# Performance work log

Measured on AMD Instinct MI355X. Metric: run time of the kernel, lower is better.

## Reference

```python
import jax, jax.numpy as jnp
import numpy as np

FORGET_BIAS = 1.0

def _lstm_step(c, h, x, W, b):
    # TF BasicLSTMCell: gates = [x; h] @ W + b, split order i, j, f, o
    z = jnp.concatenate([x, h], axis=-1) @ W + b
    i, j, f, o = jnp.split(z, 4, axis=-1)
    c_new = c * jax.nn.sigmoid(f + FORGET_BIAS) + jax.nn.sigmoid(i) * jnp.tanh(j)
    h_new = jnp.tanh(c_new) * jax.nn.sigmoid(o)
    return c_new, h_new


def setup_inputs() -> dict:
    key = jax.random.key(0)
    ks = jax.random.split(key, 8)
    V, B, T, H = 32000, 32, 256, 256
    input_data = jax.random.randint(ks[0], (B, T), 0, V, dtype=jnp.int64)
    targets = jax.random.randint(ks[1], (B, T), 0, V, dtype=jnp.int64)
    embedding = jax.random.uniform(ks[2], (V, H), jnp.float32, -1.0, 1.0)
    s = 1.0 / np.sqrt(2 * H)
    W1 = jax.random.normal(ks[3], (2 * H, 4 * H), jnp.float32) * s
    b1 = jnp.zeros((4 * H,), jnp.float32)
    W2 = jax.random.normal(ks[4], (2 * H, 4 * H), jnp.float32) * s
    b2 = jnp.zeros((4 * H,), jnp.float32)
    softmax_w = jax.random.normal(ks[5], (H, V), jnp.float32) * (1.0 / np.sqrt(H))
    softmax_b = jnp.zeros((V,), jnp.float32)
    return {"input_data": input_data, "targets": targets, "embedding": embedding,
            "W1": W1, "b1": b1, "W2": W2, "b2": b2,
            "softmax_w": softmax_w, "softmax_b": softmax_b}


def reference(input_data, targets, embedding, W1, b1, W2, b2, softmax_w, softmax_b):
    B, T = input_data.shape
    H = embedding.shape[1]
    xs = embedding[input_data].transpose(1, 0, 2)  # [T, B, H]

    def step(carry, x):
        c1, h1, c2, h2 = carry
        c1, h1 = _lstm_step(c1, h1, x, W1, b1)
        c2, h2 = _lstm_step(c2, h2, h1, W2, b2)
        return (c1, h1, c2, h2), h2

    z = jnp.zeros((B, H), xs.dtype)
    _, hs = jax.lax.scan(step, (z, z, z, z), xs)  # hs: [T, B, H]
    out = hs.transpose(1, 0, 2).reshape(-1, H)    # batch-major flatten, matches tf concat(1,...)
    logits = out @ softmax_w + softmax_b          # [B*T, V]
    logp = jax.nn.log_softmax(logits, axis=-1)
    tgt = targets.reshape(-1)
    loss = -jnp.take_along_axis(logp, tgt[:, None], axis=1)[:, 0]  # [B*T]
    cost = jnp.sum(loss) / B / T
    return cost
```

## Files before the change

kernel.cpp:

```cpp
#include <hip/hip_runtime.h>
#include <hip/hip_bf16.h>

#define Vv 32000
#define Tz 256
#define Hz 256

typedef __attribute__((ext_vector_type(8))) short short8;
typedef __attribute__((ext_vector_type(4))) float f32x4;

__device__ __forceinline__ float sigm(float x) { return 1.f / (1.f + __expf(-x)); }
__device__ __forceinline__ unsigned short f2bf(float x) {
    union { __hip_bfloat16 h; unsigned short u; } cv; cv.h = __float2bfloat16(x); return cv.u;
}

__global__ __launch_bounds__(256) void k_swt(const float* __restrict__ sw,
                                             __hip_bfloat16* __restrict__ swt) {
    __shared__ float tile[64][65];
    int kt = blockIdx.x & 3, vt = blockIdx.x >> 2;
    int k0 = kt * 64, v0 = vt * 64, tid = threadIdx.x;
#pragma unroll
    for (int p = 0; p < 16; ++p) {
        int lin = p * 256 + tid;
        int kk = lin >> 6, vvi = lin & 63;
        tile[kk][vvi] = sw[(size_t)(k0 + kk) * Vv + v0 + vvi];
    }
    __syncthreads();
#pragma unroll
    for (int p = 0; p < 16; ++p) {
        int lin = p * 256 + tid;
        int vvi = lin >> 6, kk = lin & 63;
        swt[(size_t)(v0 + vvi) * 256 + k0 + kk] = __float2bfloat16(tile[kk][vvi]);
    }
}

__global__ __launch_bounds__(64) void k_embed(const int* __restrict__ inp,
    const float* __restrict__ emb, __hip_bfloat16* __restrict__ xs) {
    int row = blockIdx.x;
    int t = row >> 5, b = row & 31;
    const float* src = emb + (size_t)inp[b * Tz + t] * Hz;
    int tid = threadIdx.x;
    float4 v = *(const float4*)&src[tid * 4];
    __hip_bfloat16* dst = xs + (size_t)row * Hz + tid * 4;
    dst[0] = __float2bfloat16(v.x); dst[1] = __float2bfloat16(v.y);
    dst[2] = __float2bfloat16(v.z); dst[3] = __float2bfloat16(v.w);
}

__device__ __forceinline__ void grid_barrier(unsigned* cnt) {
    __syncthreads();
    if (threadIdx.x == 0) {
        unsigned ticket = __hip_atomic_fetch_add(cnt, 1u, __ATOMIC_RELEASE, __HIP_MEMORY_SCOPE_AGENT);
        unsigned target = (ticket / 64u + 1u) * 64u;
        while (__hip_atomic_load(cnt, __ATOMIC_ACQUIRE, __HIP_MEMORY_SCOPE_AGENT) < target)
            __builtin_amdgcn_s_sleep(8);
    }
    __syncthreads();
}

__global__ __launch_bounds__(256) void k_lstm(
    const __hip_bfloat16* __restrict__ xs,
    const float* __restrict__ W1, const float* __restrict__ b1v,
    const float* __restrict__ W2, const float* __restrict__ b2v,
    __hip_bfloat16* __restrict__ h1buf,
    __hip_bfloat16* __restrict__ h2buf,
    float* __restrict__ houtF, __hip_bfloat16* __restrict__ houtB,
    unsigned* __restrict__ cnt)
{
    __shared__ __align__(16) unsigned short Wl[32 * 528];
    __shared__ __align__(16) unsigned short inh[32 * 272];
    __shared__ float zl[32 * 33];
    __shared__ float c_l[256];

    int bid = blockIdx.x;
    int which = bid >> 5;
    int bp = bid & 31;
    int nb = bp * 8;
    int tid = threadIdx.x;
    int w = tid >> 6, l = tid & 63, lr = l & 15, lk = l >> 4;

    const float* W    = which ? W2 : W1;
    const float* bptr = which ? b2v : b1v;

    {
        int u = tid & 31, klane = tid >> 5;
        int zc = ((u >> 3) << 8) + nb + (u & 7);
#pragma unroll 8
        for (int it = 0; it < 64; ++it) {
            int k = klane + it * 8;
            Wl[u * 528 + k] = f2bf(W[(size_t)k * 1024 + zc]);
        }
    }
    c_l[tid] = 0.f;
    float bfrag;
    {
        int r = ((w & 1) << 4) + lr;
        bfrag = bptr[((r >> 3) << 8) + nb + (r & 7)];
    }
    __syncthreads();

    float* zbuf = (float*)inh;

    for (int node = 0; node <= 256; ++node) {
        int t = which ? (node - 1) : node;
        bool valid = which ? (t >= 0) : (t < 256);
        if (valid) {
            f32x4 acc[2][2];
#pragma unroll
            for (int m = 0; m < 2; ++m)
#pragma unroll
                for (int n = 0; n < 2; ++n) acc[m][n] = (f32x4){0.f, 0.f, 0.f, 0.f};

            const unsigned short* h1p = (const unsigned short*)h1buf + ((node - 1) & 1) * 8192;
#pragma unroll
            for (int kh = 0; kh < 2; ++kh) {
                const unsigned short* src;
                if (!which) src = kh ? h1p : (const unsigned short*)xs + (size_t)t * 8192;
                else        src = kh ? (const unsigned short*)h2buf + (node & 1) * 8192 : h1p;
#pragma unroll
                for (int i = 0; i < 4; ++i) {
                    int fi = i * 256 + tid;
                    int b = fi >> 5, seg = fi & 31;
                    *(short8*)&inh[b * 272 + seg * 8] = *(const short8*)&src[fi * 8];
                }
                __syncthreads();
#pragma unroll
                for (int s = 0; s < 2; ++s) {
                    int kl = w * 64 + s * 32;
                    short8 a0 = *(const short8*)&inh[lr * 272 + kl + lk * 8];
                    short8 a1 = *(const short8*)&inh[(16 + lr) * 272 + kl + lk * 8];
                    short8 q0 = *(const short8*)&Wl[lr * 528 + kh * 256 + kl + lk * 8];
                    short8 q1 = *(const short8*)&Wl[(16 + lr) * 528 + kh * 256 + kl + lk * 8];
                    acc[0][0] = __builtin_amdgcn_mfma_f32_16x16x32_bf16(a0, q0, acc[0][0], 0, 0, 0);
                    acc[0][1] = __builtin_amdgcn_mfma_f32_16x16x32_bf16(a0, q1, acc[0][1], 0, 0, 0);
                    acc[1][0] = __builtin_amdgcn_mfma_f32_16x16x32_bf16(a1, q0, acc[1][0], 0, 0, 0);
                    acc[1][1] = __builtin_amdgcn_mfma_f32_16x16x32_bf16(a1, q1, acc[1][1], 0, 0, 0);
                }
                __syncthreads();
            }
#pragma unroll
            for (int m = 0; m < 2; ++m)
#pragma unroll
                for (int n = 0; n < 2; ++n)
                    *(f32x4*)&zbuf[((w * 4 + m * 2 + n) * 64 + l) * 4] = acc[m][n];
            __syncthreads();
            {
                int m = w >> 1, n = w & 1;
                f32x4 z = (f32x4){0.f, 0.f, 0.f, 0.f};
#pragma unroll
                for (int wv = 0; wv < 4; ++wv)
                    z += *(const f32x4*)&zbuf[((wv * 4 + m * 2 + n) * 64 + l) * 4];
                int r = n * 16 + lr;
#pragma unroll
                for (int j = 0; j < 4; ++j) {
                    int b = m * 16 + lk * 4 + j;
                    zl[b * 33 + r] = z[j] + bfrag;
                }
            }
            __syncthreads();
            {
                int jj = tid & 7, b = tid >> 3;
                float zi = zl[b * 33 + jj];
                float zj = zl[b * 33 + 8 + jj];
                float zf = zl[b * 33 + 16 + jj];
                float zo = zl[b * 33 + 24 + jj];
                float c = c_l[tid];
                float cn = c * sigm(zf + 1.f) + sigm(zi) * tanhf(zj);
                c_l[tid] = cn;
                float hv = tanhf(cn) * sigm(zo);
                int col = nb + jj;
                if (!which) {
                    ((unsigned short*)h1buf)[(node & 1) * 8192 + b * 256 + col] = f2bf(hv);
                } else {
                    ((unsigned short*)h2buf)[((node - 1) & 1) * 8192 + b * 256 + col] = f2bf(hv);
                    size_t row = (size_t)b * Tz + t;
                    houtF[row * 256 + col] = hv;
                    ((unsigned short*)houtB)[row * 256 + col] = f2bf(hv);
                }
            }
        }
        grid_barrier(cnt);
    }
}

__global__ __launch_bounds__(256) void k_gemm(const __hip_bfloat16* __restrict__ Abf,
    const __hip_bfloat16* __restrict__ Bbf, const float* __restrict__ sb,
    float* __restrict__ row_sum)
{
    __shared__ __align__(16) unsigned short As[128 * 64];
    __shared__ __align__(16) unsigned short Bs[128 * 64];
    int tid = threadIdx.x;
    size_t r0 = (size_t)blockIdx.x * 128;
    size_t c0 = (size_t)blockIdx.y * 128;
    int l = tid & 63, w = tid >> 6, lr = l & 15, lk = l >> 4;

    f32x4 acc[2][8];
#pragma unroll
    for (int m = 0; m < 2; ++m)
#pragma unroll
        for (int f = 0; f < 8; ++f) acc[m][f] = (f32x4){0.f, 0.f, 0.f, 0.f};

    const unsigned short* A = (const unsigned short*)Abf;
    const unsigned short* B = (const unsigned short*)Bbf;

    for (int kt = 0; kt < 4; ++kt) {
#pragma unroll
        for (int i = 0; i < 4; ++i) {
            int fi = i * 256 + tid;
            int row = fi >> 3, seg = fi & 7;
            int dseg = seg ^ (row & 7);
            *(short8*)&As[row * 64 + dseg * 8] =
                *(const short8*)&A[(r0 + row) * 256 + kt * 64 + seg * 8];
            *(short8*)&Bs[row * 64 + dseg * 8] =
                *(const short8*)&B[(c0 + row) * 256 + kt * 64 + seg * 8];
        }
        __syncthreads();
#pragma unroll
        for (int ks = 0; ks < 2; ++ks) {
            short8 a[2];
#pragma unroll
            for (int m = 0; m < 2; ++m) {
                int row = w * 32 + m * 16 + lr;
                a[m] = *(const short8*)&As[row * 64 + ((ks * 4 + lk) ^ (row & 7)) * 8];
            }
#pragma unroll
            for (int f = 0; f < 8; ++f) {
                int row = f * 16 + lr;
                short8 bfr = *(const short8*)&Bs[row * 64 + ((ks * 4 + lk) ^ (row & 7)) * 8];
#pragma unroll
                for (int m = 0; m < 2; ++m)
                    acc[m][f] = __builtin_amdgcn_mfma_f32_16x16x32_bf16(a[m], bfr, acc[m][f], 0, 0, 0);
            }
        }
        __syncthreads();
    }

    float sums[2][4] = {{0.f,0.f,0.f,0.f},{0.f,0.f,0.f,0.f}};
#pragma unroll
    for (int f = 0; f < 8; ++f) {
        float sbv = sb[c0 + f * 16 + lr];
#pragma unroll
        for (int m = 0; m < 2; ++m)
#pragma unroll
            for (int j = 0; j < 4; ++j) sums[m][j] += __expf(acc[m][f][j] + sbv);
    }
#pragma unroll
    for (int msk = 1; msk <= 8; msk <<= 1)
#pragma unroll
        for (int m = 0; m < 2; ++m)
#pragma unroll
            for (int j = 0; j < 4; ++j) sums[m][j] += __shfl_xor(sums[m][j], msk);
    if (lr == 0) {
#pragma unroll
        for (int m = 0; m < 2; ++m)
#pragma unroll
            for (int j = 0; j < 4; ++j)
                atomicAdd(&row_sum[r0 + w * 32 + m * 16 + lk * 4 + j], sums[m][j]);
    }
}

__global__ __launch_bounds__(256) void k_loss(const float* __restrict__ houtF,
    const float* __restrict__ sw, const float* __restrict__ sb,
    const int* __restrict__ tgts, const float* __restrict__ row_sum,
    float* __restrict__ out)
{
    int r = blockIdx.x * 256 + threadIdx.x;
    int tg = tgts[r];
    const float* h = houtF + (size_t)r * Hz;
    const float* wp = sw + tg;
    float acc = 0.f;
#pragma unroll 8
    for (int k = 0; k < Hz; ++k) acc += h[k] * wp[(size_t)k * Vv];
    float loss = logf(row_sum[r]) - (acc + sb[tg]);
#pragma unroll
    for (int m = 1; m < 64; m <<= 1) loss += __shfl_xor(loss, m);
    __shared__ float red[4];
    int l = threadIdx.x & 63, wv = threadIdx.x >> 6;
    if (l == 0) red[wv] = loss;
    __syncthreads();
    if (threadIdx.x == 0) {
        float s = red[0] + red[1] + red[2] + red[3];
        atomicAdd(out, s * (1.f / 8192.f));
    }
}

extern "C" void kernel_launch(void* const* d_in, const int* in_sizes, int n_in,
                              void* d_out, int out_size, void* d_ws, size_t ws_size,
                              hipStream_t stream)
{
    const int*   inp = (const int*)d_in[0];
    const int*   tgt = (const int*)d_in[1];
    const float* emb = (const float*)d_in[2];
    const float* W1  = (const float*)d_in[3];
    const float* b1  = (const float*)d_in[4];
    const float* W2  = (const float*)d_in[5];
    const float* b2  = (const float*)d_in[6];
    const float* sw  = (const float*)d_in[7];
    const float* sb  = (const float*)d_in[8];
    float* out = (float*)d_out;

    char* ws = (char*)d_ws;
    size_t off = 0;
    __hip_bfloat16* SWT  = (__hip_bfloat16*)(ws + off); off += (size_t)Vv * Hz * 2;
    __hip_bfloat16* XS   = (__hip_bfloat16*)(ws + off); off += (size_t)Tz * 32 * Hz * 2;
    float* HoutF         = (float*)(ws + off);          off += (size_t)8192 * Hz * 4;
    __hip_bfloat16* HoutB= (__hip_bfloat16*)(ws + off); off += (size_t)8192 * Hz * 2;
    float* row_sum       = (float*)(ws + off);          off += 8192 * 4;
    __hip_bfloat16* h1b  = (__hip_bfloat16*)(ws + off); off += 2 * 32 * Hz * 2;
    __hip_bfloat16* h2b  = (__hip_bfloat16*)(ws + off); off += 2 * 32 * Hz * 2;
    unsigned* cnt        = (unsigned*)(ws + off);       off += 16;

    hipMemsetAsync(row_sum, 0, 8192 * 4 + 2 * 32768 + 16, stream);
    hipMemsetAsync(out, 0, sizeof(float), stream);

    k_swt<<<2000, 256, 0, stream>>>(sw, SWT);
    k_embed<<<8192, 64, 0, stream>>>(inp, emb, XS);
    k_lstm<<<64, 256, 0, stream>>>(XS, W1, b1, W2, b2, h1b, h2b, HoutF, HoutB, cnt);
    k_gemm<<<dim3(64, 250), 256, 0, stream>>>(HoutB, SWT, sb, row_sum);
    k_loss<<<32, 256, 0, stream>>>(HoutF, sw, sb, tgt, row_sum, out);
}
```

Measured before the change: 1.950 ms.

## Replace atomic-counter grid barrier with per-block flags and restructure LSTM MFMA split

The single shared atomic counter barrier is replaced by a flag-array barrier. Each block stores its step number into its own padded slot, and one wavefront polls all 64 slots, so blocks no longer contend on one cache line. The recurrent matmul is also reorganised: the whole 512-wide [x;h] input is loaded once, and each wave computes a full-K 16x16 output tile. This removes the cross-wave reduction through shared memory and two of the per-step __syncthreads. The cost is that each wave's MFMA chain is longer, so the barrier latency per time step matters more.

```diff
diff --git a/kernel.cpp b/kernel.cpp
--- a/kernel.cpp
+++ b/kernel.cpp
@@ -45,17 +45,22 @@
     dst[2] = __float2bfloat16(v.z); dst[3] = __float2bfloat16(v.w);
 }
 
-__device__ __forceinline__ void grid_barrier(unsigned* cnt) {
-    __syncthreads();
-    if (threadIdx.x == 0) {
-        unsigned ticket = __hip_atomic_fetch_add(cnt, 1u, __ATOMIC_RELEASE, __HIP_MEMORY_SCOPE_AGENT);
-        unsigned target = (ticket / 64u + 1u) * 64u;
-        while (__hip_atomic_load(cnt, __ATOMIC_ACQUIRE, __HIP_MEMORY_SCOPE_AGENT) < target)
-            __builtin_amdgcn_s_sleep(8);
-    }
-    __syncthreads();
-}
-
+__device__ __forceinline__ void gbar(unsigned* flags, unsigned target, int bid) {
+    __syncthreads();
+    if (threadIdx.x < 64) {
+        if (threadIdx.x == 0)
+            __hip_atomic_store(&flags[bid * 16], target, __ATOMIC_RELEASE,
+                               __HIP_MEMORY_SCOPE_AGENT);
+        unsigned v;
+        do {
+            v = __hip_atomic_load(&flags[threadIdx.x * 16], __ATOMIC_ACQUIRE,
+                                  __HIP_MEMORY_SCOPE_AGENT);
+        } while (!__all((int)(v >= target)));
+    }
+    __syncthreads();
+}
+
+#define WSTR 520
 __global__ __launch_bounds__(256) void k_lstm(
     const __hip_bfloat16* __restrict__ xs,
     const float* __restrict__ W1, const float* __restrict__ b1v,
@@ -63,10 +68,10 @@
     __hip_bfloat16* __restrict__ h1buf,
     __hip_bfloat16* __restrict__ h2buf,
     float* __restrict__ houtF, __hip_bfloat16* __restrict__ houtB,
-    unsigned* __restrict__ cnt)
+    unsigned* __restrict__ flags)
 {
-    __shared__ __align__(16) unsigned short Wl[32 * 528];
-    __shared__ __align__(16) unsigned short inh[32 * 272];
+    __shared__ __align__(16) unsigned short Wl[32 * WSTR];
+    __shared__ __align__(16) unsigned short inh[32 * WSTR];
     __shared__ float zl[32 * 33];
     __shared__ float c_l[256];
 
@@ -86,7 +91,7 @@
 #pragma unroll 8
         for (int it = 0; it < 64; ++it) {
             int k = klane + it * 8;
-            Wl[u * 528 + k] = f2bf(W[(size_t)k * 1024 + zc]);
+            Wl[u * WSTR + k] = f2bf(W[(size_t)k * 1024 + zc]);
         }
     }
     c_l[tid] = 0.f;
@@ -97,63 +102,44 @@
     }
     __syncthreads();
 
-    float* zbuf = (float*)inh;
+    int arow = ((w >> 1) << 4) + lr;
+    int brow = ((w & 1) << 4) + lr;
 
     for (int node = 0; node <= 256; ++node) {
         int t = which ? (node - 1) : node;
         bool valid = which ? (t >= 0) : (t < 256);
         if (valid) {
-            f32x4 acc[2][2];
-#pragma unroll
-            for (int m = 0; m < 2; ++m)
-#pragma unroll
-                for (int n = 0; n < 2; ++n) acc[m][n] = (f32x4){0.f, 0.f, 0.f, 0.f};
-
             const unsigned short* h1p = (const unsigned short*)h1buf + ((node - 1) & 1) * 8192;
-#pragma unroll
-            for (int kh = 0; kh < 2; ++kh) {
-                const unsigned short* src;
-                if (!which) src = kh ? h1p : (const unsigned short*)xs + (size_t)t * 8192;
-                else        src = kh ? (const unsigned short*)h2buf + (node & 1) * 8192 : h1p;
-#pragma unroll
-                for (int i = 0; i < 4; ++i) {
-                    int fi = i * 256 + tid;
-                    int b = fi >> 5, seg = fi & 31;
-                    *(short8*)&inh[b * 272 + seg * 8] = *(const short8*)&src[fi * 8];
-                }
-                __syncthreads();
-#pragma unroll
-                for (int s = 0; s < 2; ++s) {
-                    int kl = w * 64 + s * 32;
-                    short8 a0 = *(const short8*)&inh[lr * 272 + kl + lk * 8];
-                    short8 a1 = *(const short8*)&inh[(16 + lr) * 272 + kl + lk * 8];
-                    short8 q0 = *(const short8*)&Wl[lr * 528 + kh * 256 + kl + lk * 8];
-                    short8 q1 = *(const short8*)&Wl[(16 + lr) * 528 + kh * 256 + kl + lk * 8];
-                    acc[0][0] = __builtin_amdgcn_mfma_f32_16x16x32_bf16(a0, q0, acc[0][0], 0, 0, 0);
-                    acc[0][1] = __builtin_amdgcn_mfma_f32_16x16x32_bf16(a0, q1, acc[0][1], 0, 0, 0);
-                    acc[1][0] = __builtin_amdgcn_mfma_f32_16x16x32_bf16(a1, q0, acc[1][0], 0, 0, 0);
-                    acc[1][1] = __builtin_amdgcn_mfma_f32_16x16x32_bf16(a1, q1, acc[1][1], 0, 0, 0);
-                }
-                __syncthreads();
-            }
-#pragma unroll
-            for (int m = 0; m < 2; ++m)
-#pragma unroll
-                for (int n = 0; n < 2; ++n)
-                    *(f32x4*)&zbuf[((w * 4 + m * 2 + n) * 64 + l) * 4] = acc[m][n];
+            const unsigned short *s0, *s1;
+            if (!which) { s0 = (const unsigned short*)xs + (size_t)t * 8192; s1 = h1p; }
+            else        { s0 = h1p; s1 = (const unsigned short*)h2buf + (node & 1) * 8192; }
+#pragma unroll
+            for (int i = 0; i < 8; ++i) {
+                int e = (i * 256 + tid) * 8;
+                int b = e >> 9, k = e & 511;
+                const unsigned short* sp = (k < 256) ? &s0[b * 256 + k] : &s1[b * 256 + k - 256];
+                *(short8*)&inh[b * WSTR + k] = *(const short8*)sp;
+            }
             __syncthreads();
+
+            f32x4 acc0 = (f32x4){0.f, 0.f, 0.f, 0.f};
+            f32x4 acc1 = (f32x4){0.f, 0.f, 0.f, 0.f};
+#pragma unroll
+            for (int ks = 0; ks < 16; ks += 2) {
+                short8 a0 = *(const short8*)&inh[arow * WSTR + ks * 32 + lk * 8];
+                short8 q0 = *(const short8*)&Wl[brow * WSTR + ks * 32 + lk * 8];
+                short8 a1 = *(const short8*)&inh[arow * WSTR + (ks + 1) * 32 + lk * 8];
+                short8 q1 = *(const short8*)&Wl[brow * WSTR + (ks + 1) * 32 + lk * 8];
+                acc0 = __builtin_amdgcn_mfma_f32_16x16x32_bf16(a0, q0, acc0, 0, 0, 0);
+                acc1 = __builtin_amdgcn_mfma_f32_16x16x32_bf16(a1, q1, acc1, 0, 0, 0);
+            }
+            f32x4 z = acc0 + acc1;
+
             {
                 int m = w >> 1, n = w & 1;
-                f32x4 z = (f32x4){0.f, 0.f, 0.f, 0.f};
-#pragma unroll
-                for (int wv = 0; wv < 4; ++wv)
-                    z += *(const f32x4*)&zbuf[((wv * 4 + m * 2 + n) * 64 + l) * 4];
-                int r = n * 16 + lr;
-#pragma unroll
-                for (int j = 0; j < 4; ++j) {
-                    int b = m * 16 + lk * 4 + j;
-                    zl[b * 33 + r] = z[j] + bfrag;
-                }
+#pragma unroll
+                for (int j = 0; j < 4; ++j)
+                    zl[(m * 16 + lk * 4 + j) * 33 + n * 16 + lr] = z[j] + bfrag;
             }
             __syncthreads();
             {
@@ -177,7 +163,7 @@
                 }
             }
         }
-        grid_barrier(cnt);
+        gbar(flags, (unsigned)(node + 1), bid);
     }
 }
 
@@ -306,14 +292,14 @@
     float* row_sum       = (float*)(ws + off);          off += 8192 * 4;
     __hip_bfloat16* h1b  = (__hip_bfloat16*)(ws + off); off += 2 * 32 * Hz * 2;
     __hip_bfloat16* h2b  = (__hip_bfloat16*)(ws + off); off += 2 * 32 * Hz * 2;
-    unsigned* cnt        = (unsigned*)(ws + off);       off += 16;
-
-    hipMemsetAsync(row_sum, 0, 8192 * 4 + 2 * 32768 + 16, stream);
+    unsigned* flags      = (unsigned*)(ws + off);       off += 64 * 16 * 4;
+
+    hipMemsetAsync(row_sum, 0, 8192 * 4 + 2 * 32768 + 64 * 16 * 4, stream);
     hipMemsetAsync(out, 0, sizeof(float), stream);
 
     k_swt<<<2000, 256, 0, stream>>>(sw, SWT);
     k_embed<<<8192, 64, 0, stream>>>(inp, emb, XS);
-    k_lstm<<<64, 256, 0, stream>>>(XS, W1, b1, W2, b2, h1b, h2b, HoutF, HoutB, cnt);
+    k_lstm<<<64, 256, 0, stream>>>(XS, W1, b1, W2, b2, h1b, h2b, HoutF, HoutB, flags);
     k_gemm<<<dim3(64, 250), 256, 0, stream>>>(HoutB, SWT, sb, row_sum);
     k_loss<<<32, 256, 0, stream>>>(HoutF, sw, sb, tgt, row_sum, out);
 }
```

Measured after the change: 1.561 ms. -19.9%, faster.
